# Kernel tuning notes

Hardware: AMD Instinct MI355X
Metric: run time of the kernel (lower is better)

## Reference

```python
import jax, jax.numpy as jnp
import numpy as np

HOPS = 2
BN_EPS = 1e-5


def _glorot(key, shape):
    fan_in = shape[-2]
    bound = 1.0 / np.sqrt(fan_in)
    return jax.random.uniform(key, shape, jnp.float32, -bound, bound)


def setup_inputs() -> dict:
    key = jax.random.key(0)
    ks = jax.random.split(key, 12)
    n, e = 50000, 800000
    in_c, hid, out_c = 128, 96, 64
    x = jax.random.normal(ks[0], (n, in_c), jnp.float32)
    edge_index = jax.random.randint(ks[1], (2, e), 0, n, jnp.int32)
    # MixHopLayer 0: hops+1 linears in_c -> hid (stacked)
    conv0_W = _glorot(ks[2], (HOPS + 1, in_c, hid))
    conv0_b = jnp.zeros((HOPS + 1, hid), jnp.float32)
    # MixHopLayer 1: hops+1 linears hid*(hops+1) -> out_c
    conv1_W = _glorot(ks[3], (HOPS + 1, hid * (HOPS + 1), out_c))
    conv1_b = jnp.zeros((HOPS + 1, out_c), jnp.float32)
    # BatchNorm1d(hid*(hops+1)) eval-mode params/buffers
    w = hid * (HOPS + 1)
    bn_gamma = jnp.ones((w,), jnp.float32)
    bn_beta = jnp.zeros((w,), jnp.float32)
    bn_mean = 0.1 * jax.random.normal(ks[4], (w,), jnp.float32)
    bn_var = jnp.ones((w,), jnp.float32) + 0.1 * jax.random.uniform(ks[5], (w,))
    # final projection out_c*(hops+1) -> out_c
    fp_W = _glorot(ks[6], (out_c * (HOPS + 1), out_c))
    fp_b = jnp.zeros((out_c,), jnp.float32)
    return dict(x=x, edge_index=edge_index, conv0_W=conv0_W, conv0_b=conv0_b,
                conv1_W=conv1_W, conv1_b=conv1_b, bn_gamma=bn_gamma, bn_beta=bn_beta,
                bn_mean=bn_mean, bn_var=bn_var, fp_W=fp_W, fp_b=fp_b)


def _gcn_norm(edge_index, n):
    # PyG gcn_norm with add_self_loops=True, improved=False, symmetric norm.
    row, col = edge_index[0], edge_index[1]
    loop = jnp.arange(n, dtype=edge_index.dtype)
    row = jnp.concatenate([row, loop])
    col = jnp.concatenate([col, loop])
    deg = jax.ops.segment_sum(jnp.ones_like(col, jnp.float32), col, num_segments=n)
    dinv = jnp.where(deg > 0, jax.lax.rsqrt(deg), 0.0)
    w = dinv[row] * dinv[col]
    return row, col, w


def _spmm_adj_t(row, col, w, x, n):
    # adj_t = SparseTensor(row=col, col=row, value=w): out[col] += w * x[row]
    return jax.ops.segment_sum(w[:, None] * x[row], col, num_segments=n)


def _mixhop_layer(x, W, b, row, col, w, n):
    xs = [x @ W[0] + b[0]]
    for j in range(1, HOPS + 1):
        xj = x @ W[j] + b[j]
        for _ in range(j):
            xj = _spmm_adj_t(row, col, w, xj, n)
        xs.append(xj)
    return jnp.concatenate(xs, axis=1)


def reference(x, edge_index, conv0_W, conv0_b, conv1_W, conv1_b,
              bn_gamma, bn_beta, bn_mean, bn_var, fp_W, fp_b):
    n = x.shape[0]
    row, col, w = _gcn_norm(edge_index, n)
    h = _mixhop_layer(x, conv0_W, conv0_b, row, col, w, n)
    # BatchNorm1d (eval) + ReLU; dropout is identity in eval
    h = bn_gamma * (h - bn_mean) * jax.lax.rsqrt(bn_var + BN_EPS) + bn_beta
    h = jax.nn.relu(h)
    h = _mixhop_layer(h, conv1_W, conv1_b, row, col, w, n)
    return h @ fp_W + fp_b
```

## Files before the change

### kernel.cpp

```cpp
#include <hip/hip_runtime.h>

#define IN_C 128
#define HID 96
#define OUT_C 64
#define W0C 288
#define W1C 192
#define CAP 5120
#define EPB 1024

typedef __bf16 bf16x8v __attribute__((ext_vector_type(8)));
typedef float  f32x4v  __attribute__((ext_vector_type(4)));


__global__ void k_combo_prep(const float* __restrict__ x, __bf16* __restrict__ xb, int n8,
                             const float* __restrict__ W0, const float* __restrict__ W1,
                             const float* __restrict__ Wf,
                             const float* __restrict__ gamma, const float* __restrict__ beta,
                             const float* __restrict__ mean, const float* __restrict__ var,
                             __bf16* __restrict__ w0t, __bf16* __restrict__ w1t,
                             __bf16* __restrict__ wft,
                             float* __restrict__ scale, float* __restrict__ shift,
                             int* __restrict__ zp, int nz,
                             int CB, int PB) {
    int b = blockIdx.x;
    if (b < CB) {
        int i = b * 256 + threadIdx.x;
        if (i >= n8) return;
        bf16x8v o;
#pragma unroll
        for (int q = 0; q < 8; q++) o[q] = (__bf16)x[i * 8 + q];
        *(bf16x8v*)(xb + (size_t)i * 8) = o;
    } else if (b < CB + PB) {
        const int T0 = 3 * IN_C * HID;
        const int T1 = 3 * W0C * OUT_C;
        const int T2 = W1C * OUT_C;
        int i = (b - CB) * 256 + threadIdx.x;
        if (i < T0) {
            int kn = IN_C * HID;
            int j = i / kn, r = i % kn;
            int k = r / HID, nn = r % HID;
            w0t[(size_t)j * kn + (size_t)nn * IN_C + k] = (__bf16)W0[i];
        } else if (i < T0 + T1) {
            int ii = i - T0;
            int kn = W0C * OUT_C;
            int j = ii / kn, r = ii % kn;
            int k = r / OUT_C, nn = r % OUT_C;
            w1t[(size_t)j * kn + (size_t)nn * W0C + k] = (__bf16)W1[ii];
        } else if (i < T0 + T1 + T2) {
            int ii = i - T0 - T1;
            int k = ii / OUT_C, nn = ii % OUT_C;
            wft[(size_t)nn * W1C + k] = (__bf16)Wf[ii];
        } else if (i < T0 + T1 + T2 + W0C) {
            int ii = i - T0 - T1 - T2;
            float s = gamma[ii] * rsqrtf(var[ii] + 1e-5f);
            scale[ii] = s;
            shift[ii] = beta[ii] - mean[ii] * s;
        }
    } else {
        int i = (b - CB - PB) * 256 + threadIdx.x;
        if (i < nz) zp[i] = 0;
    }
}

__global__ __launch_bounds__(256) void k_mega0(
        const int* __restrict__ row, const int* __restrict__ col,
        int* __restrict__ bcur ,
        int* __restrict__ binned, int e, int SB,
        const __bf16* __restrict__ xb, const __bf16* __restrict__ w0t ,
        const float* __restrict__ bias , __bf16* __restrict__ h,
        const float* __restrict__ scale, const float* __restrict__ shift, int M) {
    const int RS = 104;
    __shared__ __bf16 tile[128 * RS];
    int tid = threadIdx.x;
    if ((int)blockIdx.x < SB) {
        int* hist  = (int*)tile;
        int* basep = hist + 256;
        int e0 = blockIdx.x * EPB;
        int cnt = min(EPB, e - e0);
        hist[tid] = 0;
        __syncthreads();
        int rr[4], cc[4], rk[4];
#pragma unroll
        for (int k = 0; k < 4; k++) {
            int idx = tid + k * 256;
            if (idx < cnt) {
                rr[k] = row[e0 + idx];
                cc[k] = col[e0 + idx];
                rk[k] = atomicAdd(&hist[cc[k] >> 8], 1);
            }
        }
        __syncthreads();
        {
            int hv = hist[tid];
            if (hv > 0) basep[tid] = atomicAdd(&bcur[tid * 16], hv);
        }
        __syncthreads();
#pragma unroll
        for (int k = 0; k < 4; k++) {
            int idx = tid + k * 256;
            if (idx < cnt) {
                int b = cc[k] >> 8;
                int pos = basep[b] + rk[k];
                if (pos < CAP)
                    binned[(size_t)b * CAP + pos] = (rr[k] << 8) | (cc[k] & 255);
            }
        }
        return;
    }
    int wave = tid >> 6, lane = tid & 63;
    int ln = lane & 15, quad = lane >> 4;
    int rowBase = (blockIdx.x - SB) * 128;
    int waveRow = wave * 16;
    f32x4v acc[2][6];
#pragma unroll
    for (int u = 0; u < 2; u++)
#pragma unroll
        for (int t = 0; t < 6; t++) acc[u][t] = (f32x4v){0.f, 0.f, 0.f, 0.f};
    const __bf16* arow0 = xb + (size_t)(rowBase + waveRow + ln) * IN_C + quad * 8;
    const __bf16* arow1 = arow0 + (size_t)64 * IN_C;
#pragma unroll
    for (int k = 0; k < 4; k++) {
        bf16x8v a0 = *(const bf16x8v*)(arow0 + k * 32);
        bf16x8v a1 = *(const bf16x8v*)(arow1 + k * 32);
#pragma unroll
        for (int c = 0; c < 6; c++) {
            bf16x8v b = *(const bf16x8v*)(w0t + (size_t)(c * 16 + ln) * IN_C + k * 32 + quad * 8);
            acc[0][c] = __builtin_amdgcn_mfma_f32_16x16x32_bf16(a0, b, acc[0][c], 0, 0, 0);
            acc[1][c] = __builtin_amdgcn_mfma_f32_16x16x32_bf16(a1, b, acc[1][c], 0, 0, 0);
        }
    }
#pragma unroll
    for (int u = 0; u < 2; u++)
#pragma unroll
        for (int r = 0; r < 4; r++) {
            int lr = u * 64 + waveRow + quad * 4 + r;
#pragma unroll
            for (int c = 0; c < 6; c++) {
                int col2 = c * 16 + ln;
                float v = acc[u][c][r] + bias[col2];
                v = fmaxf(v * scale[col2] + shift[col2], 0.f);
                tile[lr * RS + col2] = (__bf16)v;
            }
        }
    __syncthreads();
#pragma unroll
    for (int s = 0; s < 6; s++) {
        int idx = tid + s * 256;
        int r = idx / 12, c8 = idx % 12;
        int grow = rowBase + r;
        if (grow < M)
            *(bf16x8v*)(h + (size_t)grow * W0C + c8 * 8) =
                *(const bf16x8v*)(tile + r * RS + c8 * 8);
    }
}

__global__ __launch_bounds__(256) void k_bucket_all(
        const int* __restrict__ binned, const int* __restrict__ bcur,
        float* __restrict__ dinv, int* __restrict__ csrs, int* __restrict__ row_ptr,
        int n, int nb) {
    __shared__ int s_pack[CAP];
    __shared__ int s_ofs[256];
    __shared__ int lcur[256];
    __shared__ int s_scan[256];
    int tid = threadIdx.x;
    int b = blockIdx.x;
    int node0 = b << 8;
    int v = (tid < nb) ? bcur[tid * 16] : 0;
    s_scan[tid] = v;
    __syncthreads();
    for (int o = 1; o < 256; o <<= 1) {
        int u = (tid >= o) ? s_scan[tid - o] : 0;
        __syncthreads();
        s_scan[tid] += u;
        __syncthreads();
    }
    int base = (b > 0) ? s_scan[b - 1] : 0;
    int cnt = min(bcur[b * 16], CAP);
    const int* bin = binned + (size_t)b * CAP;
    lcur[tid] = 0;
    __syncthreads();
    for (int t = tid; t < cnt; t += 256)
        atomicAdd(&lcur[bin[t] & 255], 1);
    __syncthreads();
    int cdeg = lcur[tid];
    int node = node0 + tid;
    if (node < n) dinv[node] = rsqrtf((float)(cdeg + 1));
    s_ofs[tid] = cdeg;
    __syncthreads();
    for (int o = 1; o < 256; o <<= 1) {
        int u = (tid >= o) ? s_ofs[tid - o] : 0;
        __syncthreads();
        s_ofs[tid] += u;
        __syncthreads();
    }
    int nodeOfs = s_ofs[tid] - cdeg;
    if (node < n) {
        row_ptr[node] = base + nodeOfs;
        if (node == n - 1) row_ptr[n] = base + nodeOfs + cdeg;
    }
    lcur[tid] = 0;
    __syncthreads();
    for (int t = tid; t < cnt; t += 256)
        atomicAdd(&lcur[bin[t] >> 16], 1);
    __syncthreads();
    {
        int vv = lcur[tid];
        s_ofs[tid] = vv;
        __syncthreads();
        for (int o = 1; o < 256; o <<= 1) {
            int u = (tid >= o) ? s_ofs[tid - o] : 0;
            __syncthreads();
            s_ofs[tid] += u;
            __syncthreads();
        }
        lcur[tid] = s_ofs[tid] - vv;
    }
    __syncthreads();
    for (int t = tid; t < cnt; t += 256) {
        int p = bin[t];
        int pos = atomicAdd(&lcur[p >> 16], 1);
        s_pack[pos] = p;
    }
    __syncthreads();
    s_ofs[tid] = nodeOfs;
    lcur[tid] = 0;
    __syncthreads();
    for (int t = tid; t < cnt; t += 256) {
        int p = s_pack[t];
        int r = p >> 8;
        int local = p & 255;
        int pos = s_ofs[local] + atomicAdd(&lcur[local], 1);
        csrs[base + pos] = r;
    }
}


__global__ __launch_bounds__(256) void k_mf_l0b(
        const __bf16* __restrict__ s1, const __bf16* __restrict__ w0t,
        const float* __restrict__ bias , const float* __restrict__ arow,
        __bf16* __restrict__ h, __bf16* __restrict__ tp,
        const float* __restrict__ scale, const float* __restrict__ shift, int M) {
    const int RS = 104;
    __shared__ __bf16 tile[64 * RS];
    int tid = threadIdx.x;
    int wave = tid >> 6, lane = tid & 63;
    int ln = lane & 15, quad = lane >> 4;
    int rowBase = blockIdx.x * 64;
    int waveRow = wave * 16;
    const __bf16* w1p = w0t + (size_t)1 * HID * IN_C;
    const __bf16* w2p = w0t + (size_t)2 * HID * IN_C;
    f32x4v acc[2][6];
#pragma unroll
    for (int j = 0; j < 2; j++)
#pragma unroll
        for (int t = 0; t < 6; t++) acc[j][t] = (f32x4v){0.f, 0.f, 0.f, 0.f};
    const __bf16* arow0 = s1 + (size_t)(rowBase + waveRow + ln) * IN_C + quad * 8;
#pragma unroll
    for (int k = 0; k < 4; k++) {
        bf16x8v a0 = *(const bf16x8v*)(arow0 + k * 32);
#pragma unroll
        for (int c = 0; c < 6; c++) {
            bf16x8v b1 = *(const bf16x8v*)(w1p + (size_t)(c * 16 + ln) * IN_C + k * 32 + quad * 8);
            bf16x8v b2 = *(const bf16x8v*)(w2p + (size_t)(c * 16 + ln) * IN_C + k * 32 + quad * 8);
            acc[0][c] = __builtin_amdgcn_mfma_f32_16x16x32_bf16(a0, b1, acc[0][c], 0, 0, 0);
            acc[1][c] = __builtin_amdgcn_mfma_f32_16x16x32_bf16(a0, b2, acc[1][c], 0, 0, 0);
        }
    }
    float avs[4];
#pragma unroll
    for (int r = 0; r < 4; r++)
        avs[r] = arow[rowBase + waveRow + quad * 4 + r];
#pragma unroll
    for (int jj = 0; jj < 2; jj++) {
        const float* bj = bias + (jj + 1) * HID;
#pragma unroll
        for (int r = 0; r < 4; r++) {
            int lr = waveRow + quad * 4 + r;
            float av = avs[r];
#pragma unroll
            for (int c = 0; c < 6; c++) {
                int col = c * 16 + ln;
                float v = acc[jj][c][r] + av * bj[col];
                if (jj == 0) v = fmaxf(v * scale[HID + col] + shift[HID + col], 0.f);
                tile[lr * RS + col] = (__bf16)v;
            }
        }
        __syncthreads();
#pragma unroll
        for (int s = 0; s < 3; s++) {
            int idx = tid + s * 256;
            int r = idx / 12, c8 = idx % 12;
            int grow = rowBase + r;
            if (grow < M) {
                __bf16* dst = (jj == 0) ? (h + (size_t)grow * W0C + HID)
                                        : (tp + (size_t)grow * HID);
                *(bf16x8v*)(dst + c8 * 8) = *(const bf16x8v*)(tile + r * RS + c8 * 8);
            }
        }
        __syncthreads();
    }
}

__global__ __launch_bounds__(256) void k_mf_l1m(
        const __bf16* __restrict__ hb, const __bf16* __restrict__ w1t ,
        const float* __restrict__ bias ,
        __bf16* __restrict__ g, __bf16* __restrict__ u12, int M) {
    const int RS = 72;
    __shared__ __bf16 tile[64 * RS];
    int tid = threadIdx.x;
    int wave = tid >> 6, lane = tid & 63;
    int ln = lane & 15, quad = lane >> 4;
    int rowBase = blockIdx.x * 64;
    int waveRow = wave * 16;
    f32x4v acc[3][4];
#pragma unroll
    for (int j = 0; j < 3; j++)
#pragma unroll
        for (int t = 0; t < 4; t++) acc[j][t] = (f32x4v){0.f, 0.f, 0.f, 0.f};
    const __bf16* arow0 = hb + (size_t)(rowBase + waveRow + ln) * W0C + quad * 8;
#pragma unroll
    for (int k = 0; k < 9; k++) {
        bf16x8v a0 = *(const bf16x8v*)(arow0 + k * 32);
#pragma unroll
        for (int c = 0; c < 4; c++) {
#pragma unroll
            for (int j = 0; j < 3; j++) {
                bf16x8v b = *(const bf16x8v*)(w1t + (size_t)j * OUT_C * W0C +
                                              (size_t)(c * 16 + ln) * W0C + k * 32 + quad * 8);
                acc[j][c] = __builtin_amdgcn_mfma_f32_16x16x32_bf16(a0, b, acc[j][c], 0, 0, 0);
            }
        }
    }
#pragma unroll
    for (int j = 0; j < 3; j++) {
        const float* bj = bias + j * OUT_C;
#pragma unroll
        for (int r = 0; r < 4; r++) {
            int lr = waveRow + quad * 4 + r;
#pragma unroll
            for (int c = 0; c < 4; c++) {
                int col = c * 16 + ln;
                tile[lr * RS + col] = (__bf16)(acc[j][c][r] + bj[col]);
            }
        }
        __syncthreads();
        __bf16* dst = (j == 0) ? g : u12;
        int ld = (j == 0) ? W1C : 128;
        int c0 = (j == 2) ? OUT_C : 0;
#pragma unroll
        for (int s = 0; s < 2; s++) {
            int idx = tid + s * 256;
            int r = idx / 8, c8 = idx % 8;
            int grow = rowBase + r;
            if (grow < M)
                *(bf16x8v*)(dst + (size_t)grow * ld + c0 + c8 * 8) =
                    *(const bf16x8v*)(tile + r * RS + c8 * 8);
        }
        __syncthreads();
    }
}

__global__ __launch_bounds__(256) void k_mf_fin(
        const __bf16* __restrict__ gb, const __bf16* __restrict__ wft ,
        const float* __restrict__ bias, float* __restrict__ out, int M) {
    const int RS = 68;
    __shared__ float tile[128 * RS];
    int tid = threadIdx.x;
    int wave = tid >> 6, lane = tid & 63;
    int ln = lane & 15, quad = lane >> 4;
    int rowBase = blockIdx.x * 128;
    int waveRow = wave * 16;
    f32x4v acc[2][4];
#pragma unroll
    for (int u = 0; u < 2; u++)
#pragma unroll
        for (int t = 0; t < 4; t++) acc[u][t] = (f32x4v){0.f, 0.f, 0.f, 0.f};
    const __bf16* arow0 = gb + (size_t)(rowBase + waveRow + ln) * W1C + quad * 8;
    const __bf16* arow1 = arow0 + (size_t)64 * W1C;
#pragma unroll
    for (int k = 0; k < 6; k++) {
        bf16x8v a0 = *(const bf16x8v*)(arow0 + k * 32);
        bf16x8v a1 = *(const bf16x8v*)(arow1 + k * 32);
#pragma unroll
        for (int c = 0; c < 4; c++) {
            bf16x8v b = *(const bf16x8v*)(wft + (size_t)(c * 16 + ln) * W1C + k * 32 + quad * 8);
            acc[0][c] = __builtin_amdgcn_mfma_f32_16x16x32_bf16(a0, b, acc[0][c], 0, 0, 0);
            acc[1][c] = __builtin_amdgcn_mfma_f32_16x16x32_bf16(a1, b, acc[1][c], 0, 0, 0);
        }
    }
#pragma unroll
    for (int u = 0; u < 2; u++)
#pragma unroll
        for (int r = 0; r < 4; r++) {
            int lr = u * 64 + waveRow + quad * 4 + r;
#pragma unroll
            for (int c = 0; c < 4; c++) {
                int col = c * 16 + ln;
                tile[lr * RS + col] = acc[u][c][r] + bias[col];
            }
        }
    __syncthreads();
#pragma unroll
    for (int s = 0; s < 8; s++) {
        int idx = tid + s * 256;
        int r = idx / 16, c4 = idx % 16;
        int grow = rowBase + r;
        if (grow < M)
            *(float4*)(out + (size_t)grow * OUT_C + c4 * 4) =
                *(const float4*)(tile + r * RS + c4 * 4);
    }
}

template <int C8, int NPB, bool BNRELU, bool AROW>
__global__ void k_spmm(const __bf16* __restrict__ xin, int ldx,
                       __bf16* __restrict__ xout, int ldo,
                       const int* __restrict__ row_ptr,
                       const int* __restrict__ csrs,
                       const float* __restrict__ dinv, int n,
                       const float* __restrict__ scale, const float* __restrict__ shift,
                       int chan0, float* __restrict__ arow) {
    int c8 = threadIdx.x % C8;
    int nl = threadIdx.x / C8;
    int node = blockIdx.x * NPB + nl;
    if (node >= n) return;
    float di = dinv[node];
    float lw = di * di;
    float acc[8];
    {
        bf16x8v v = *(const bf16x8v*)(xin + (size_t)node * ldx + c8 * 8);
#pragma unroll
        for (int q = 0; q < 8; q++) acc[q] = lw * (float)v[q];
    }
    float aw = lw;
    int start = row_ptr[node];
    int cnt = row_ptr[node + 1] - start;
    const int* cp = csrs + start;
    int k = 0;
    for (; k + 4 <= cnt; k += 4) {
        int s0 = cp[k + 0], s1 = cp[k + 1], s2 = cp[k + 2], s3 = cp[k + 3];
        float w0 = dinv[s0] * di, w1 = dinv[s1] * di;
        float w2 = dinv[s2] * di, w3 = dinv[s3] * di;
        bf16x8v v0 = *(const bf16x8v*)(xin + (size_t)s0 * ldx + c8 * 8);
        bf16x8v v1 = *(const bf16x8v*)(xin + (size_t)s1 * ldx + c8 * 8);
        bf16x8v v2 = *(const bf16x8v*)(xin + (size_t)s2 * ldx + c8 * 8);
        bf16x8v v3 = *(const bf16x8v*)(xin + (size_t)s3 * ldx + c8 * 8);
#pragma unroll
        for (int q = 0; q < 8; q++)
            acc[q] += w0 * (float)v0[q] + w1 * (float)v1[q] +
                      w2 * (float)v2[q] + w3 * (float)v3[q];
        if (AROW) aw += w0 + w1 + w2 + w3;
    }
    for (; k < cnt; k++) {
        int s = cp[k];
        float w = dinv[s] * di;
        bf16x8v xv = *(const bf16x8v*)(xin + (size_t)s * ldx + c8 * 8);
#pragma unroll
        for (int q = 0; q < 8; q++) acc[q] += w * (float)xv[q];
        if (AROW) aw += w;
    }
    if (AROW && c8 == 0) arow[node] = aw;
    bf16x8v o;
#pragma unroll
    for (int q = 0; q < 8; q++) {
        float v = acc[q];
        if (BNRELU) {
            int ch = chan0 + c8 * 8 + q;
            v = fmaxf(v * scale[ch] + shift[ch], 0.f);
        }
        o[q] = (__bf16)v;
    }
    *(bf16x8v*)(xout + (size_t)node * ldo + c8 * 8) = o;
}

template <int C8, int SPLIT, int NPB, bool BNA, bool BNB>
__global__ void k_spmm2(const __bf16* __restrict__ xin, int ldx,
                        __bf16* __restrict__ dstA, int ldA, int chanA,
                        __bf16* __restrict__ dstB, int ldB, int chanB,
                        const int* __restrict__ row_ptr,
                        const int* __restrict__ csrs,
                        const float* __restrict__ dinv, int n,
                        const float* __restrict__ scale, const float* __restrict__ shift) {
    int c8 = threadIdx.x % C8;
    int nl = threadIdx.x / C8;
    int node = blockIdx.x * NPB + nl;
    if (node >= n) return;
    float di = dinv[node];
    float lw = di * di;
    float acc[8];
    {
        bf16x8v v = *(const bf16x8v*)(xin + (size_t)node * ldx + c8 * 8);
#pragma unroll
        for (int q = 0; q < 8; q++) acc[q] = lw * (float)v[q];
    }
    int start = row_ptr[node];
    int cnt = row_ptr[node + 1] - start;
    const int* cp = csrs + start;
    int k = 0;
    for (; k + 4 <= cnt; k += 4) {
        int s0 = cp[k + 0], s1 = cp[k + 1], s2 = cp[k + 2], s3 = cp[k + 3];
        float w0 = dinv[s0] * di, w1 = dinv[s1] * di;
        float w2 = dinv[s2] * di, w3 = dinv[s3] * di;
        bf16x8v v0 = *(const bf16x8v*)(xin + (size_t)s0 * ldx + c8 * 8);
        bf16x8v v1 = *(const bf16x8v*)(xin + (size_t)s1 * ldx + c8 * 8);
        bf16x8v v2 = *(const bf16x8v*)(xin + (size_t)s2 * ldx + c8 * 8);
        bf16x8v v3 = *(const bf16x8v*)(xin + (size_t)s3 * ldx + c8 * 8);
#pragma unroll
        for (int q = 0; q < 8; q++)
            acc[q] += w0 * (float)v0[q] + w1 * (float)v1[q] +
                      w2 * (float)v2[q] + w3 * (float)v3[q];
    }
    for (; k < cnt; k++) {
        int s = cp[k];
        float w = dinv[s] * di;
        bf16x8v xv = *(const bf16x8v*)(xin + (size_t)s * ldx + c8 * 8);
#pragma unroll
        for (int q = 0; q < 8; q++) acc[q] += w * (float)xv[q];
    }
    bool isA = c8 < SPLIT;
    __bf16* dst = isA ? dstA : dstB;
    int ld   = isA ? ldA : ldB;
    int lc8  = isA ? c8 : c8 - SPLIT;
    int chan = isA ? chanA : chanB;
    bool bn  = isA ? BNA : BNB;
    bf16x8v o;
#pragma unroll
    for (int q = 0; q < 8; q++) {
        float v = acc[q];
        if (bn) {
            int ch = chan + lc8 * 8 + q;
            v = fmaxf(v * scale[ch] + shift[ch], 0.f);
        }
        o[q] = (__bf16)v;
    }
    *(bf16x8v*)(dst + (size_t)node * ld + lc8 * 8) = o;
}


extern "C" void kernel_launch(void* const* d_in, const int* in_sizes, int n_in,
                              void* d_out, int out_size, void* d_ws, size_t ws_size,
                              hipStream_t stream) {
    const int n = in_sizes[0] / IN_C;
    const int e = in_sizes[1] / 2;

    const float* x    = (const float*)d_in[0];
    const int*   ei   = (const int*)d_in[1];
    const float* W0   = (const float*)d_in[2];
    const float* b0   = (const float*)d_in[3];
    const float* W1   = (const float*)d_in[4];
    const float* b1   = (const float*)d_in[5];
    const float* bn_g = (const float*)d_in[6];
    const float* bn_b = (const float*)d_in[7];
    const float* bn_m = (const float*)d_in[8];
    const float* bn_v = (const float*)d_in[9];
    const float* Wf   = (const float*)d_in[10];
    const float* bf   = (const float*)d_in[11];
    float* out = (float*)d_out;

    const int* e_row = ei;
    const int* e_col = ei + e;

    char* ws = (char*)d_ws;
    size_t off = 0;
    auto alloc = [&](size_t bytes) -> void* {
        void* p = ws + off;
        off += (bytes + 255) & ~(size_t)255;
        return p;
    };
    const int NP = n + 128;
    int nb = (n + 255) / 256;

    int*    bcur    = (int*)alloc((size_t)256 * 16 * 4);
    int*    row_ptr = (int*)alloc((size_t)(n + 1) * 4);
    float*  dinv    = (float*)alloc((size_t)n * 4);
    float*  arow    = (float*)alloc((size_t)NP * 4);
    int*    binned  = (int*)alloc((size_t)nb * CAP * 4);
    int*    csrs    = (int*)alloc((size_t)e * 4);
    float*  bnscale = (float*)alloc(W0C * 4);
    float*  bnshift = (float*)alloc(W0C * 4);
    __bf16* xb  = (__bf16*)alloc((size_t)NP * IN_C * 2);
    __bf16* w0t = (__bf16*)alloc((size_t)3 * HID * IN_C * 2);
    __bf16* w1t = (__bf16*)alloc((size_t)3 * OUT_C * W0C * 2);
    __bf16* wft = (__bf16*)alloc((size_t)OUT_C * W1C * 2);
    __bf16* s1  = (__bf16*)alloc((size_t)NP * 128 * 2);
    __bf16* tp  = (__bf16*)alloc((size_t)NP * HID * 2);
    __bf16* h   = (__bf16*)alloc((size_t)NP * W0C * 2);
    __bf16* g   = (__bf16*)alloc((size_t)NP * W1C * 2);
    __bf16* u12 = s1;
    __bf16* up  = tp;

    int n8 = n * IN_C / 8;
    int nz = 256 * 16;
    int ptotal = 3 * IN_C * HID + 3 * W0C * OUT_C + W1C * OUT_C + W0C;
    int CB = (n8 + 255) / 256;
    int PB = (ptotal + 255) / 256;
    int ZB = (nz + 255) / 256;
    k_combo_prep<<<dim3(CB + PB + ZB), dim3(256), 0, stream>>>(
        x, xb, n8, W0, W1, Wf, bn_g, bn_b, bn_m, bn_v,
        w0t, w1t, wft, bnscale, bnshift, bcur, nz, CB, PB);

    int SB = (e + EPB - 1) / EPB;
    int GG = (n + 127) / 128;
    k_mega0<<<dim3(SB + GG), dim3(256), 0, stream>>>(
        e_row, e_col, bcur, binned, e, SB,
        xb, w0t, b0, h, bnscale, bnshift, n);

    k_bucket_all<<<dim3(nb), dim3(256), 0, stream>>>(binned, bcur, dinv, csrs,
                                                     row_ptr, n, nb);

    dim3 g64((n + 63) / 64);

    k_spmm<16, 16, false, true><<<dim3((n + 15) / 16), dim3(256), 0, stream>>>(
        xb, IN_C, s1, 128, row_ptr, csrs, dinv, n, nullptr, nullptr, 0, arow);
    k_mf_l0b<<<g64, dim3(256), 0, stream>>>(s1, w0t, b0, arow, h, tp, bnscale, bnshift, n);
    k_spmm<12, 16, true, false><<<dim3((n + 15) / 16), dim3(192), 0, stream>>>(
        tp, HID, h + 2 * HID, W0C, row_ptr, csrs, dinv, n, bnscale, bnshift,
        2 * HID, nullptr);

    k_mf_l1m<<<g64, dim3(256), 0, stream>>>(h, w1t, b1, g, u12, n);

    k_spmm2<16, 8, 16, false, false><<<dim3((n + 15) / 16), dim3(256), 0, stream>>>(
        u12, 128, g + OUT_C, W1C, 0, up, OUT_C, 0,
        row_ptr, csrs, dinv, n, nullptr, nullptr);
    k_spmm<8, 32, false, false><<<dim3((n + 31) / 32), dim3(256), 0, stream>>>(
        up, OUT_C, g + 2 * OUT_C, W1C, row_ptr, csrs, dinv, n, nullptr, nullptr,
        0, nullptr);

    k_mf_fin<<<dim3((n + 127) / 128), dim3(256), 0, stream>>>(g, wft, bf, out, n);
}
```

Before: 316.4 us.

## Rotate SpMM neighbor traversal start by block and fuse CSR-build histogram passes

In the SpMM kernels, each block binary-searches its sorted neighbor list for a rotation point chosen from blockIdx modulo 8. It then walks the neighbors from there and wraps around, so concurrently running blocks touch different source-node ranges. This aims to spread gather traffic across memory channels and L2 sets, and it costs a binary search per node and a changed accumulation order. Separately, the CSR-build kernel merges its two histogram passes over the binned edges into one pass with two LDS atomics.

```diff
diff --git a/kernel.cpp b/kernel.cpp
--- a/kernel.cpp
+++ b/kernel.cpp
@@ -177,12 +177,16 @@
     int base = (b > 0) ? s_scan[b - 1] : 0;
     int cnt = min(bcur[b * 16], CAP);
     const int* bin = binned + (size_t)b * CAP;
+    s_scan[tid] = 0;
     lcur[tid] = 0;
     __syncthreads();
-    for (int t = tid; t < cnt; t += 256)
-        atomicAdd(&lcur[bin[t] & 255], 1);
-    __syncthreads();
-    int cdeg = lcur[tid];
+    for (int t = tid; t < cnt; t += 256) {
+        int p = bin[t];
+        atomicAdd(&s_scan[p & 255], 1);
+        atomicAdd(&lcur[p >> 16], 1);
+    }
+    __syncthreads();
+    int cdeg = s_scan[tid];
     int node = node0 + tid;
     if (node < n) dinv[node] = rsqrtf((float)(cdeg + 1));
     s_ofs[tid] = cdeg;
@@ -198,10 +202,6 @@
         row_ptr[node] = base + nodeOfs;
         if (node == n - 1) row_ptr[n] = base + nodeOfs + cdeg;
     }
-    lcur[tid] = 0;
-    __syncthreads();
-    for (int t = tid; t < cnt; t += 256)
-        atomicAdd(&lcur[bin[t] >> 16], 1);
     __syncthreads();
     {
         int vv = lcur[tid];
@@ -435,28 +435,42 @@
     int start = row_ptr[node];
     int cnt = row_ptr[node + 1] - start;
     const int* cp = csrs + start;
-    int k = 0;
-    for (; k + 4 <= cnt; k += 4) {
-        int s0 = cp[k + 0], s1 = cp[k + 1], s2 = cp[k + 2], s3 = cp[k + 3];
-        float w0 = dinv[s0] * di, w1 = dinv[s1] * di;
-        float w2 = dinv[s2] * di, w3 = dinv[s3] * di;
-        bf16x8v v0 = *(const bf16x8v*)(xin + (size_t)s0 * ldx + c8 * 8);
-        bf16x8v v1 = *(const bf16x8v*)(xin + (size_t)s1 * ldx + c8 * 8);
-        bf16x8v v2 = *(const bf16x8v*)(xin + (size_t)s2 * ldx + c8 * 8);
-        bf16x8v v3 = *(const bf16x8v*)(xin + (size_t)s3 * ldx + c8 * 8);
-#pragma unroll
-        for (int q = 0; q < 8; q++)
-            acc[q] += w0 * (float)v0[q] + w1 * (float)v1[q] +
-                      w2 * (float)v2[q] + w3 * (float)v3[q];
-        if (AROW) aw += w0 + w1 + w2 + w3;
-    }
-    for (; k < cnt; k++) {
-        int s = cp[k];
-        float w = dinv[s] * di;
-        bf16x8v xv = *(const bf16x8v*)(xin + (size_t)s * ldx + c8 * 8);
-#pragma unroll
-        for (int q = 0; q < 8; q++) acc[q] += w * (float)xv[q];
-        if (AROW) aw += w;
+    int rb = (blockIdx.x & 7) * 25;
+    int split = 0;
+    if (rb) {
+        int lo = 0, hi = cnt;
+        while (lo < hi) {
+            int mid = (lo + hi) >> 1;
+            if ((cp[mid] >> 8) >= rb) hi = mid; else lo = mid + 1;
+        }
+        split = lo;
+    }
+#pragma unroll
+    for (int sgi = 0; sgi < 2; sgi++) {
+        int k    = sgi ? 0 : split;
+        int kend = sgi ? split : cnt;
+        for (; k + 4 <= kend; k += 4) {
+            int s0 = cp[k + 0], s1 = cp[k + 1], s2 = cp[k + 2], s3 = cp[k + 3];
+            float w0 = dinv[s0] * di, w1 = dinv[s1] * di;
+            float w2 = dinv[s2] * di, w3 = dinv[s3] * di;
+            bf16x8v v0 = *(const bf16x8v*)(xin + (size_t)s0 * ldx + c8 * 8);
+            bf16x8v v1 = *(const bf16x8v*)(xin + (size_t)s1 * ldx + c8 * 8);
+            bf16x8v v2 = *(const bf16x8v*)(xin + (size_t)s2 * ldx + c8 * 8);
+            bf16x8v v3 = *(const bf16x8v*)(xin + (size_t)s3 * ldx + c8 * 8);
+#pragma unroll
+            for (int q = 0; q < 8; q++)
+                acc[q] += w0 * (float)v0[q] + w1 * (float)v1[q] +
+                          w2 * (float)v2[q] + w3 * (float)v3[q];
+            if (AROW) aw += w0 + w1 + w2 + w3;
+        }
+        for (; k < kend; k++) {
+            int s = cp[k];
+            float w = dinv[s] * di;
+            bf16x8v xv = *(const bf16x8v*)(xin + (size_t)s * ldx + c8 * 8);
+#pragma unroll
+            for (int q = 0; q < 8; q++) acc[q] += w * (float)xv[q];
+            if (AROW) aw += w;
+        }
     }
     if (AROW && c8 == 0) arow[node] = aw;
     bf16x8v o;
@@ -495,26 +509,40 @@
     int start = row_ptr[node];
     int cnt = row_ptr[node + 1] - start;
     const int* cp = csrs + start;
-    int k = 0;
-    for (; k + 4 <= cnt; k += 4) {
-        int s0 = cp[k + 0], s1 = cp[k + 1], s2 = cp[k + 2], s3 = cp[k + 3];
-        float w0 = dinv[s0] * di, w1 = dinv[s1] * di;
-        float w2 = dinv[s2] * di, w3 = dinv[s3] * di;
-        bf16x8v v0 = *(const bf16x8v*)(xin + (size_t)s0 * ldx + c8 * 8);
-        bf16x8v v1 = *(const bf16x8v*)(xin + (size_t)s1 * ldx + c8 * 8);
-        bf16x8v v2 = *(const bf16x8v*)(xin + (size_t)s2 * ldx + c8 * 8);
-        bf16x8v v3 = *(const bf16x8v*)(xin + (size_t)s3 * ldx + c8 * 8);
-#pragma unroll
-        for (int q = 0; q < 8; q++)
-            acc[q] += w0 * (float)v0[q] + w1 * (float)v1[q] +
-                      w2 * (float)v2[q] + w3 * (float)v3[q];
-    }
-    for (; k < cnt; k++) {
-        int s = cp[k];
-        float w = dinv[s] * di;
-        bf16x8v xv = *(const bf16x8v*)(xin + (size_t)s * ldx + c8 * 8);
-#pragma unroll
-        for (int q = 0; q < 8; q++) acc[q] += w * (float)xv[q];
+    int rb = (blockIdx.x & 7) * 25;
+    int split = 0;
+    if (rb) {
+        int lo = 0, hi = cnt;
+        while (lo < hi) {
+            int mid = (lo + hi) >> 1;
+            if ((cp[mid] >> 8) >= rb) hi = mid; else lo = mid + 1;
+        }
+        split = lo;
+    }
+#pragma unroll
+    for (int sgi = 0; sgi < 2; sgi++) {
+        int k    = sgi ? 0 : split;
+        int kend = sgi ? split : cnt;
+        for (; k + 4 <= kend; k += 4) {
+            int s0 = cp[k + 0], s1 = cp[k + 1], s2 = cp[k + 2], s3 = cp[k + 3];
+            float w0 = dinv[s0] * di, w1 = dinv[s1] * di;
+            float w2 = dinv[s2] * di, w3 = dinv[s3] * di;
+            bf16x8v v0 = *(const bf16x8v*)(xin + (size_t)s0 * ldx + c8 * 8);
+            bf16x8v v1 = *(const bf16x8v*)(xin + (size_t)s1 * ldx + c8 * 8);
+            bf16x8v v2 = *(const bf16x8v*)(xin + (size_t)s2 * ldx + c8 * 8);
+            bf16x8v v3 = *(const bf16x8v*)(xin + (size_t)s3 * ldx + c8 * 8);
+#pragma unroll
+            for (int q = 0; q < 8; q++)
+                acc[q] += w0 * (float)v0[q] + w1 * (float)v1[q] +
+                          w2 * (float)v2[q] + w3 * (float)v3[q];
+        }
+        for (; k < kend; k++) {
+            int s = cp[k];
+            float w = dinv[s] * di;
+            bf16x8v xv = *(const bf16x8v*)(xin + (size_t)s * ldx + c8 * 8);
+#pragma unroll
+            for (int q = 0; q < 8; q++) acc[q] += w * (float)xv[q];
+        }
     }
     bool isA = c8 < SPLIT;
     __bf16* dst = isA ? dstA : dstB;
```

After: 326.2 us. 1.03x slower.

## Fold final projection into layer-1 GEMM and reassociate hops via Horner

Applied to the files above, without the earlier changes.

Layer 1 now multiplies each hop's output by its slice of the final projection weight inside the GEMM kernel, giving three 64-wide per-hop projections. The hop propagation is reassociated as A(A·p2 + p1) + p0, so the sparse passes work on 64 channels instead of 128+64, and the separate final GEMM kernel is removed. The bucket kernel also counts both histograms in one pass over the bins. The intermediate bf16 rounding of the projected values adds some numerical error.

```diff
diff --git a/kernel.cpp b/kernel.cpp
--- a/kernel.cpp
+++ b/kernel.cpp
@@ -177,12 +177,16 @@
     int base = (b > 0) ? s_scan[b - 1] : 0;
     int cnt = min(bcur[b * 16], CAP);
     const int* bin = binned + (size_t)b * CAP;
+    s_scan[tid] = 0;
     lcur[tid] = 0;
     __syncthreads();
-    for (int t = tid; t < cnt; t += 256)
-        atomicAdd(&lcur[bin[t] & 255], 1);
-    __syncthreads();
-    int cdeg = lcur[tid];
+    for (int t = tid; t < cnt; t += 256) {
+        int p = bin[t];
+        atomicAdd(&s_scan[p & 255], 1);
+        atomicAdd(&lcur[p >> 16], 1);
+    }
+    __syncthreads();
+    int cdeg = s_scan[tid];
     int node = node0 + tid;
     if (node < n) dinv[node] = rsqrtf((float)(cdeg + 1));
     s_ofs[tid] = cdeg;
@@ -198,10 +202,6 @@
         row_ptr[node] = base + nodeOfs;
         if (node == n - 1) row_ptr[n] = base + nodeOfs + cdeg;
     }
-    lcur[tid] = 0;
-    __syncthreads();
-    for (int t = tid; t < cnt; t += 256)
-        atomicAdd(&lcur[bin[t] >> 16], 1);
     __syncthreads();
     {
         int vv = lcur[tid];
@@ -301,10 +301,12 @@
     }
 }
 
-__global__ __launch_bounds__(256) void k_mf_l1m(
+__global__ __launch_bounds__(256) void k_mf_l1pf(
         const __bf16* __restrict__ hb, const __bf16* __restrict__ w1t ,
         const float* __restrict__ bias ,
-        __bf16* __restrict__ g, __bf16* __restrict__ u12, int M) {
+        const __bf16* __restrict__ wft , const float* __restrict__ bf,
+        __bf16* __restrict__ p0b, __bf16* __restrict__ p1b, __bf16* __restrict__ p2b,
+        int M) {
     const int RS = 72;
     __shared__ __bf16 tile[64 * RS];
     int tid = threadIdx.x;
@@ -343,82 +345,53 @@
                 tile[lr * RS + col] = (__bf16)(acc[j][c][r] + bj[col]);
             }
         }
-        __syncthreads();
-        __bf16* dst = (j == 0) ? g : u12;
-        int ld = (j == 0) ? W1C : 128;
-        int c0 = (j == 2) ? OUT_C : 0;
+        f32x4v acc2[4];
+#pragma unroll
+        for (int t = 0; t < 4; t++) acc2[t] = (f32x4v){0.f, 0.f, 0.f, 0.f};
+#pragma unroll
+        for (int kk = 0; kk < 2; kk++) {
+            bf16x8v a = *(const bf16x8v*)(tile + (waveRow + ln) * RS + kk * 32 + quad * 8);
+#pragma unroll
+            for (int c = 0; c < 4; c++) {
+                bf16x8v b = *(const bf16x8v*)(wft + (size_t)(c * 16 + ln) * W1C +
+                                              j * 64 + kk * 32 + quad * 8);
+                acc2[c] = __builtin_amdgcn_mfma_f32_16x16x32_bf16(a, b, acc2[c], 0, 0, 0);
+            }
+        }
+#pragma unroll
+        for (int r = 0; r < 4; r++) {
+            int lr = waveRow + quad * 4 + r;
+#pragma unroll
+            for (int c = 0; c < 4; c++) {
+                int col = c * 16 + ln;
+                float v = acc2[c][r] + (j == 0 ? bf[col] : 0.f);
+                tile[lr * RS + col] = (__bf16)v;
+            }
+        }
+        __syncthreads();
+        __bf16* dst = (j == 0) ? p0b : ((j == 1) ? p1b : p2b);
 #pragma unroll
         for (int s = 0; s < 2; s++) {
             int idx = tid + s * 256;
             int r = idx / 8, c8 = idx % 8;
             int grow = rowBase + r;
             if (grow < M)
-                *(bf16x8v*)(dst + (size_t)grow * ld + c0 + c8 * 8) =
+                *(bf16x8v*)(dst + (size_t)grow * 64 + c8 * 8) =
                     *(const bf16x8v*)(tile + r * RS + c8 * 8);
         }
         __syncthreads();
     }
 }
 
-__global__ __launch_bounds__(256) void k_mf_fin(
-        const __bf16* __restrict__ gb, const __bf16* __restrict__ wft ,
-        const float* __restrict__ bias, float* __restrict__ out, int M) {
-    const int RS = 68;
-    __shared__ float tile[128 * RS];
-    int tid = threadIdx.x;
-    int wave = tid >> 6, lane = tid & 63;
-    int ln = lane & 15, quad = lane >> 4;
-    int rowBase = blockIdx.x * 128;
-    int waveRow = wave * 16;
-    f32x4v acc[2][4];
-#pragma unroll
-    for (int u = 0; u < 2; u++)
-#pragma unroll
-        for (int t = 0; t < 4; t++) acc[u][t] = (f32x4v){0.f, 0.f, 0.f, 0.f};
-    const __bf16* arow0 = gb + (size_t)(rowBase + waveRow + ln) * W1C + quad * 8;
-    const __bf16* arow1 = arow0 + (size_t)64 * W1C;
-#pragma unroll
-    for (int k = 0; k < 6; k++) {
-        bf16x8v a0 = *(const bf16x8v*)(arow0 + k * 32);
-        bf16x8v a1 = *(const bf16x8v*)(arow1 + k * 32);
-#pragma unroll
-        for (int c = 0; c < 4; c++) {
-            bf16x8v b = *(const bf16x8v*)(wft + (size_t)(c * 16 + ln) * W1C + k * 32 + quad * 8);
-            acc[0][c] = __builtin_amdgcn_mfma_f32_16x16x32_bf16(a0, b, acc[0][c], 0, 0, 0);
-            acc[1][c] = __builtin_amdgcn_mfma_f32_16x16x32_bf16(a1, b, acc[1][c], 0, 0, 0);
-        }
-    }
-#pragma unroll
-    for (int u = 0; u < 2; u++)
-#pragma unroll
-        for (int r = 0; r < 4; r++) {
-            int lr = u * 64 + waveRow + quad * 4 + r;
-#pragma unroll
-            for (int c = 0; c < 4; c++) {
-                int col = c * 16 + ln;
-                tile[lr * RS + col] = acc[u][c][r] + bias[col];
-            }
-        }
-    __syncthreads();
-#pragma unroll
-    for (int s = 0; s < 8; s++) {
-        int idx = tid + s * 256;
-        int r = idx / 16, c4 = idx % 16;
-        int grow = rowBase + r;
-        if (grow < M)
-            *(float4*)(out + (size_t)grow * OUT_C + c4 * 4) =
-                *(const float4*)(tile + r * RS + c4 * 4);
-    }
-}
-
-template <int C8, int NPB, bool BNRELU, bool AROW>
+template <int C8, int NPB, bool BNRELU, bool AROW, bool ADDIN>
 __global__ void k_spmm(const __bf16* __restrict__ xin, int ldx,
                        __bf16* __restrict__ xout, int ldo,
                        const int* __restrict__ row_ptr,
                        const int* __restrict__ csrs,
                        const float* __restrict__ dinv, int n,
                        const float* __restrict__ scale, const float* __restrict__ shift,
-                       int chan0, float* __restrict__ arow) {
+                       int chan0, float* __restrict__ arow,
+                       const __bf16* __restrict__ addin) {
     int c8 = threadIdx.x % C8;
     int nl = threadIdx.x / C8;
     int node = blockIdx.x * NPB + nl;
@@ -459,10 +432,13 @@
         if (AROW) aw += w;
     }
     if (AROW && c8 == 0) arow[node] = aw;
+    bf16x8v ai;
+    if (ADDIN) ai = *(const bf16x8v*)(addin + (size_t)node * 64 + c8 * 8);
     bf16x8v o;
 #pragma unroll
     for (int q = 0; q < 8; q++) {
         float v = acc[q];
+        if (ADDIN) v += (float)ai[q];
         if (BNRELU) {
             int ch = chan0 + c8 * 8 + q;
             v = fmaxf(v * scale[ch] + shift[ch], 0.f);
@@ -472,23 +448,20 @@
     *(bf16x8v*)(xout + (size_t)node * ldo + c8 * 8) = o;
 }
 
-template <int C8, int SPLIT, int NPB, bool BNA, bool BNB>
-__global__ void k_spmm2(const __bf16* __restrict__ xin, int ldx,
-                        __bf16* __restrict__ dstA, int ldA, int chanA,
-                        __bf16* __restrict__ dstB, int ldB, int chanB,
-                        const int* __restrict__ row_ptr,
-                        const int* __restrict__ csrs,
-                        const float* __restrict__ dinv, int n,
-                        const float* __restrict__ scale, const float* __restrict__ shift) {
-    int c8 = threadIdx.x % C8;
-    int nl = threadIdx.x / C8;
-    int node = blockIdx.x * NPB + nl;
+__global__ void k_spmm_fin(const __bf16* __restrict__ qin ,
+                           const __bf16* __restrict__ p0b ,
+                           const int* __restrict__ row_ptr, const int* __restrict__ csrs,
+                           const float* __restrict__ dinv, int n,
+                           float* __restrict__ out) {
+    int c8 = threadIdx.x % 8;
+    int nl = threadIdx.x / 8;
+    int node = blockIdx.x * 32 + nl;
     if (node >= n) return;
     float di = dinv[node];
     float lw = di * di;
     float acc[8];
     {
-        bf16x8v v = *(const bf16x8v*)(xin + (size_t)node * ldx + c8 * 8);
+        bf16x8v v = *(const bf16x8v*)(qin + (size_t)node * 64 + c8 * 8);
 #pragma unroll
         for (int q = 0; q < 8; q++) acc[q] = lw * (float)v[q];
     }
@@ -500,10 +473,10 @@
         int s0 = cp[k + 0], s1 = cp[k + 1], s2 = cp[k + 2], s3 = cp[k + 3];
         float w0 = dinv[s0] * di, w1 = dinv[s1] * di;
         float w2 = dinv[s2] * di, w3 = dinv[s3] * di;
-        bf16x8v v0 = *(const bf16x8v*)(xin + (size_t)s0 * ldx + c8 * 8);
-        bf16x8v v1 = *(const bf16x8v*)(xin + (size_t)s1 * ldx + c8 * 8);
-        bf16x8v v2 = *(const bf16x8v*)(xin + (size_t)s2 * ldx + c8 * 8);
-        bf16x8v v3 = *(const bf16x8v*)(xin + (size_t)s3 * ldx + c8 * 8);
+        bf16x8v v0 = *(const bf16x8v*)(qin + (size_t)s0 * 64 + c8 * 8);
+        bf16x8v v1 = *(const bf16x8v*)(qin + (size_t)s1 * 64 + c8 * 8);
+        bf16x8v v2 = *(const bf16x8v*)(qin + (size_t)s2 * 64 + c8 * 8);
+        bf16x8v v3 = *(const bf16x8v*)(qin + (size_t)s3 * 64 + c8 * 8);
 #pragma unroll
         for (int q = 0; q < 8; q++)
             acc[q] += w0 * (float)v0[q] + w1 * (float)v1[q] +
@@ -512,27 +485,18 @@
     for (; k < cnt; k++) {
         int s = cp[k];
         float w = dinv[s] * di;
-        bf16x8v xv = *(const bf16x8v*)(xin + (size_t)s * ldx + c8 * 8);
+        bf16x8v xv = *(const bf16x8v*)(qin + (size_t)s * 64 + c8 * 8);
 #pragma unroll
         for (int q = 0; q < 8; q++) acc[q] += w * (float)xv[q];
     }
-    bool isA = c8 < SPLIT;
-    __bf16* dst = isA ? dstA : dstB;
-    int ld   = isA ? ldA : ldB;
-    int lc8  = isA ? c8 : c8 - SPLIT;
-    int chan = isA ? chanA : chanB;
-    bool bn  = isA ? BNA : BNB;
-    bf16x8v o;
-#pragma unroll
-    for (int q = 0; q < 8; q++) {
-        float v = acc[q];
-        if (bn) {
-            int ch = chan + lc8 * 8 + q;
-            v = fmaxf(v * scale[ch] + shift[ch], 0.f);
-        }
-        o[q] = (__bf16)v;
-    }
-    *(bf16x8v*)(dst + (size_t)node * ld + lc8 * 8) = o;
+    bf16x8v pv = *(const bf16x8v*)(p0b + (size_t)node * 64 + c8 * 8);
+    f32x4v o0, o1;
+#pragma unroll
+    for (int q = 0; q < 4; q++) o0[q] = acc[q] + (float)pv[q];
+#pragma unroll
+    for (int q = 0; q < 4; q++) o1[q] = acc[4 + q] + (float)pv[4 + q];
+    *(f32x4v*)(out + (size_t)node * OUT_C + c8 * 8) = o0;
+    *(f32x4v*)(out + (size_t)node * OUT_C + c8 * 8 + 4) = o1;
 }
 
 
@@ -584,9 +548,10 @@
     __bf16* s1  = (__bf16*)alloc((size_t)NP * 128 * 2);
     __bf16* tp  = (__bf16*)alloc((size_t)NP * HID * 2);
     __bf16* h   = (__bf16*)alloc((size_t)NP * W0C * 2);
-    __bf16* g   = (__bf16*)alloc((size_t)NP * W1C * 2);
-    __bf16* u12 = s1;
-    __bf16* up  = tp;
+    __bf16* p0b = (__bf16*)alloc((size_t)NP * OUT_C * 2);
+    __bf16* p1b = (__bf16*)alloc((size_t)NP * OUT_C * 2);
+    __bf16* p2b = (__bf16*)alloc((size_t)NP * OUT_C * 2);
+    __bf16* qb  = tp;
 
     int n8 = n * IN_C / 8;
     int nz = 256 * 16;
@@ -609,21 +574,18 @@
 
     dim3 g64((n + 63) / 64);
 
-    k_spmm<16, 16, false, true><<<dim3((n + 15) / 16), dim3(256), 0, stream>>>(
-        xb, IN_C, s1, 128, row_ptr, csrs, dinv, n, nullptr, nullptr, 0, arow);
+    k_spmm<16, 16, false, true, false><<<dim3((n + 15) / 16), dim3(256), 0, stream>>>(
+        xb, IN_C, s1, 128, row_ptr, csrs, dinv, n, nullptr, nullptr, 0, arow, nullptr);
     k_mf_l0b<<<g64, dim3(256), 0, stream>>>(s1, w0t, b0, arow, h, tp, bnscale, bnshift, n);
-    k_spmm<12, 16, true, false><<<dim3((n + 15) / 16), dim3(192), 0, stream>>>(
+    k_spmm<12, 16, true, false, false><<<dim3((n + 15) / 16), dim3(192), 0, stream>>>(
         tp, HID, h + 2 * HID, W0C, row_ptr, csrs, dinv, n, bnscale, bnshift,
-        2 * HID, nullptr);
-
-    k_mf_l1m<<<g64, dim3(256), 0, stream>>>(h, w1t, b1, g, u12, n);
-
-    k_spmm2<16, 8, 16, false, false><<<dim3((n + 15) / 16), dim3(256), 0, stream>>>(
-        u12, 128, g + OUT_C, W1C, 0, up, OUT_C, 0,
-        row_ptr, csrs, dinv, n, nullptr, nullptr);
-    k_spmm<8, 32, false, false><<<dim3((n + 31) / 32), dim3(256), 0, stream>>>(
-        up, OUT_C, g + 2 * OUT_C, W1C, row_ptr, csrs, dinv, n, nullptr, nullptr,
-        0, nullptr);
-
-    k_mf_fin<<<dim3((n + 127) / 128), dim3(256), 0, stream>>>(g, wft, bf, out, n);
-}
+        2 * HID, nullptr, nullptr);
+
+    k_mf_l1pf<<<g64, dim3(256), 0, stream>>>(h, w1t, b1, wft, bf, p0b, p1b, p2b, n);
+
+    k_spmm<8, 32, false, false, true><<<dim3((n + 31) / 32), dim3(256), 0, stream>>>(
+        p2b, OUT_C, qb, OUT_C, row_ptr, csrs, dinv, n, nullptr, nullptr, 0,
+        nullptr, p1b);
+    k_spmm_fin<<<dim3((n + 31) / 32), dim3(256), 0, stream>>>(
+        qb, p0b, row_ptr, csrs, dinv, n, out);
+}
```

Measured after the change: 304.1 us. -3.9%, faster.
